# Performance work log

Measured on AMD Instinct MI355X. Metric: run time of the kernel, lower is better.

The kernel has to match this reference:

```python
import jax, jax.numpy as jnp
import numpy as np
from jax import lax

B, C, L = 32, 8, 4096
K, S = 128, 64  # num_shapelets, shapelets_size


def setup_inputs() -> dict:
    key = jax.random.key(0)
    kx, ks = jax.random.split(key)
    x = jax.random.normal(kx, (B, C, L), dtype=jnp.float32)
    shapelets = jax.random.normal(ks, (C, K, S), dtype=jnp.float32)
    return {"x": x, "shapelets": shapelets}


def reference(x, shapelets):
    # x: (B, C, L); shapelets: (C, K, S)
    # Equivalent to: unfold -> cdist(p=2) -> sum over channels -> min over windows.
    # Use the ||a-b||^2 = ||a||^2 + ||b||^2 - 2 a.b expansion so the unfolded
    # (B, C, W, S) tensor is never materialized; cross-terms via grouped conv.
    Bc, Cc, Lc = x.shape
    _, Kc, Sc = shapelets.shape
    dn = ("NCH", "OIH", "NCH")
    # cross[b, c*K+k, w] = sum_s x[b,c,w+s] * shapelets[c,k,s]
    rhs = shapelets.reshape(Cc * Kc, 1, Sc)
    cross = lax.conv_general_dilated(x, rhs, (1,), "VALID",
                                     feature_group_count=Cc,
                                     dimension_numbers=dn)  # (B, C*K, W)
    W = cross.shape[-1]
    cross = cross.reshape(Bc, Cc, Kc, W)
    # sliding window squared norms of x: conv of x^2 with ones kernel per channel
    ones = jnp.ones((Cc, 1, Sc), x.dtype)
    xnorm = lax.conv_general_dilated(x * x, ones, (1,), "VALID",
                                     feature_group_count=Cc,
                                     dimension_numbers=dn)  # (B, C, W)
    snorm = jnp.sum(shapelets * shapelets, axis=-1)  # (C, K)
    d2 = xnorm[:, :, None, :] + snorm[None, :, :, None] - 2.0 * cross  # (B,C,K,W)
    d = jnp.sqrt(jnp.maximum(d2, 1e-12))
    summed = jnp.sum(d, axis=1, keepdims=True)  # (B, 1, K, W)
    return jnp.min(summed, axis=3)  # (B, 1, K)
```

## Files before the change

### kernel.cpp

```cpp
#include <hip/hip_runtime.h>


typedef short short8 __attribute__((ext_vector_type(8)));
typedef float f32x4 __attribute__((ext_vector_type(4)));

constexpr int Bn = 32, Cn = 8, Ln = 4096, Kn = 128, Sn = 64;
constexpr int Wn = Ln - Sn + 1;
constexpr int WT = 128;
constexpr int NWT = (Wn + WT - 1) / WT;
constexpr int BDIM = 256;

typedef const __attribute__((address_space(1))) unsigned int gas_u32;
typedef __attribute__((address_space(3))) unsigned int las_u32;

__device__ __forceinline__ unsigned int f2bf(float f) {
  unsigned int u = __float_as_uint(f);
  u += 0x7FFFu + ((u >> 16) & 1u);
  return u >> 16;
}

__global__ void prep_kernel(const float* __restrict__ sh,
                            unsigned int* __restrict__ out,
                            unsigned short* __restrict__ hbf,
                            float* __restrict__ snorm) {
  int gid = blockIdx.x * blockDim.x + threadIdx.x;
  out[gid] = 0x7F7FFFFFu;
  if (gid < Cn * Kn) {
    const float4* row = (const float4*)(sh + (size_t)gid * Sn);
    char* rowb = (char*)hbf + (size_t)gid * (Sn * 2);
    const unsigned int sw = (gid & 7u) << 4;
    float a = 0.f;
    #pragma unroll
    for (int i = 0; i < 16; ++i) {
      float4 v = row[i];
      a += v.x * v.x + v.y * v.y + v.z * v.z + v.w * v.w;
      unsigned int p0 = f2bf(-2.f * v.x) | (f2bf(-2.f * v.y) << 16);
      unsigned int p1 = f2bf(-2.f * v.z) | (f2bf(-2.f * v.w) << 16);
      *(uint2*)(rowb + ((8u * i) ^ sw)) = make_uint2(p0, p1);
    }
    snorm[gid] = a;
  }
}

__launch_bounds__(BDIM, 2)
__global__ void med_kernel(const float* __restrict__ x,
                           const unsigned short* __restrict__ hbf,
                           const float* __restrict__ snorm,
                           unsigned int* __restrict__ out) {
  constexpr int XRS = 200;
  __shared__ __align__(16) unsigned short Xr[2][8 * XRS];
  __shared__ __align__(16) unsigned short Bs[2][Kn * Sn];
  __shared__ __align__(16) float xnormC[Cn * WT];
  __shared__ __align__(16) float snormC[Cn * Kn];

  const int tid  = threadIdx.x;
  const int b    = blockIdx.y;
  const int w0   = blockIdx.x * WT;
  const int lane = tid & 63;
  const int wv   = tid >> 6;
  const int quad = lane >> 4;
  const int n16  = lane & 15;
  const int wbase = wv * 32;

  const float* xb = x + (size_t)b * Cn * Ln;

  auto stage_b = [&](int bufi, int c) {
    const char* src = (const char*)hbf + (size_t)c * (Kn * Sn * 2);
    char* dst = (char*)&Bs[bufi][0];
    #pragma unroll
    for (int rep = 0; rep < 4; ++rep) {
      int q16 = (tid + rep * BDIM) * 16;
      __builtin_amdgcn_global_load_lds((gas_u32*)(src + q16), (las_u32*)(dst + q16),
                                       16, 0, 0);
    }
  };

  int x_lds[3], x_g[3];
  #pragma unroll
  for (int rep = 0; rep < 3; ++rep) {
    int pid = tid + rep * BDIM;
    int r = pid / 96;
    int p = pid - r * 96;
    x_lds[rep] = r * XRS + 2 * p;
    x_g[rep] = w0 + r + 2 * p;
  }
  float xf[3][2];
  auto load_x = [&](int c) {
    const float* xc = xb + (size_t)c * Ln;
    #pragma unroll
    for (int rep = 0; rep < 3; ++rep) {
      int i0 = x_g[rep];
      xf[rep][0] = (i0 < Ln) ? xc[i0] : 0.f;
      xf[rep][1] = (i0 + 1 < Ln) ? xc[i0 + 1] : 0.f;
    }
  };
  auto write_x = [&](int bufi) {
    #pragma unroll
    for (int rep = 0; rep < 3; ++rep)
      *(unsigned int*)(&Xr[bufi][x_lds[rep]]) =
          f2bf(xf[rep][0]) | (f2bf(xf[rep][1]) << 16);
  };

  ((float4*)snormC)[tid] = ((const float4*)snorm)[tid];

  stage_b(0, 0);
  load_x(0);

  {
    int c  = tid >> 5;
    int m0 = (tid & 31) * 4;
    const float* xc = xb + c * Ln;
    auto xq = [&](int i) -> float {
      float v = (i < Ln) ? xc[i] : 0.f;
      return v * v;
    };
    float s0 = 0.f;
    for (int s = 0; s < Sn; ++s) s0 += xq(w0 + m0 + s);
    float s1 = s0 - xq(w0 + m0 + 0) + xq(w0 + m0 + 64);
    float s2 = s1 - xq(w0 + m0 + 1) + xq(w0 + m0 + 65);
    float s3 = s2 - xq(w0 + m0 + 2) + xq(w0 + m0 + 66);
    xnormC[c * WT + m0 + 0] = s0;
    xnormC[c * WT + m0 + 1] = s1;
    xnormC[c * WT + m0 + 2] = s2;
    xnormC[c * WT + m0 + 3] = s3;
  }
  write_x(0);
  __syncthreads();

  float dist[2][8][4] = {};

  for (int c = 0; c < Cn; ++c) {
    const int buf = c & 1;

    if (c + 1 < Cn) {
      stage_b(buf ^ 1, c + 1);
      load_x(c + 1);
    }

    float4 xn[2];
    #pragma unroll
    for (int mt = 0; mt < 2; ++mt)
      xn[mt] = *(const float4*)(&xnormC[c * WT + wbase + mt * 16 + quad * 4]);

    short8 af[2][2];
    #pragma unroll
    for (int mt = 0; mt < 2; ++mt)
      #pragma unroll
      for (int ks = 0; ks < 2; ++ks) {
        int i = wbase + mt * 16 + n16 + ks * 32 + quad * 8;
        af[mt][ks] = *(const short8*)(&Xr[buf][(i & 7) * XRS + (i >> 3) * 8]);
      }

    const char* bsb = (const char*)&Bs[buf][0];
    #pragma unroll
    for (int pass = 0; pass < 2; ++pass) {
      #pragma unroll
      for (int nt = 0; nt < 4; ++nt) {
        int ksh = pass * 64 + nt * 16 + n16;
        float sn = snormC[c * Kn + ksh];
        int boff = (ksh * 128 + quad * 16) ^ ((ksh & 7) << 4);
        short8 b0 = *(const short8*)(bsb + (boff ^ 0));
        short8 b1 = *(const short8*)(bsb + (boff ^ 64));
        #pragma unroll
        for (int mt = 0; mt < 2; ++mt) {
          f32x4 acc;
          #pragma unroll
          for (int rg = 0; rg < 4; ++rg) acc[rg] = xn[mt][rg] + sn;
          acc = __builtin_amdgcn_mfma_f32_16x16x32_bf16(af[mt][0], b0, acc, 0, 0, 0);
          acc = __builtin_amdgcn_mfma_f32_16x16x32_bf16(af[mt][1], b1, acc, 0, 0, 0);
          #pragma unroll
          for (int rg = 0; rg < 4; ++rg)
            dist[mt][pass * 4 + nt][rg] += __builtin_amdgcn_sqrtf(acc[rg]);
        }
      }
    }

    if (c + 1 < Cn) write_x(buf ^ 1);
    __syncthreads();
  }

  const int wql = w0 + wbase + quad * 4;
  #pragma unroll
  for (int nt2 = 0; nt2 < 8; ++nt2) {
    float v = 3.4e38f;
    #pragma unroll
    for (int mt = 0; mt < 2; ++mt)
      #pragma unroll
      for (int rg = 0; rg < 4; ++rg) {
        int wg = wql + mt * 16 + rg;
        float d = (wg < Wn) ? dist[mt][nt2][rg] : 3.4e38f;
        v = fminf(v, d);
      }
    v = fminf(v, __shfl_xor(v, 16, 64));
    v = fminf(v, __shfl_xor(v, 32, 64));
    if (lane < 16)
      atomicMin(&out[b * Kn + nt2 * 16 + n16], __float_as_uint(v));
  }
}

extern "C" void kernel_launch(void* const* d_in, const int* in_sizes, int n_in,
                              void* d_out, int out_size, void* d_ws, size_t ws_size,
                              hipStream_t stream) {
  const float* x  = (const float*)d_in[0];
  const float* sh = (const float*)d_in[1];
  unsigned int* out = (unsigned int*)d_out;
  unsigned short* hbf = (unsigned short*)d_ws;
  float* snorm = (float*)((char*)d_ws + (size_t)Cn * Kn * Sn * 2);
  hipLaunchKernelGGL(prep_kernel, dim3(16), dim3(256), 0, stream, sh, out, hbf, snorm);
  hipLaunchKernelGGL(med_kernel, dim3(NWT, Bn), dim3(BDIM), 0, stream, x, hbf, snorm, out);
}
```

Baseline: 110.4 us.

## Halve window tile and split shapelet halves across waves for higher occupancy

Shrinks the per-block window tile from 128 to 64. The four waves are now split as 2 window rows × 2 shapelet halves instead of 4 window rows that each cover all 128 shapelets. This halves the per-wave accumulator registers and lets launch bounds request 3 blocks per SIMD, with twice as many blocks in the grid. The trade-off is that every block still stages the full bf16 shapelet matrix per channel, so shapelet LDS and global traffic per output window roughly doubles, and the sliding-norm prologue overhead is amortised over fewer windows.

```diff
diff --git a/kernel.cpp b/kernel.cpp
--- a/kernel.cpp
+++ b/kernel.cpp
@@ -6,9 +6,12 @@
 
 constexpr int Bn = 32, Cn = 8, Ln = 4096, Kn = 128, Sn = 64;
 constexpr int Wn = Ln - Sn + 1;
-constexpr int WT = 128;
+constexpr int WT = 64;
 constexpr int NWT = (Wn + WT - 1) / WT;
 constexpr int BDIM = 256;
+constexpr int XRS = 136;
+constexpr int PPR = 64;
+constexpr int PAIRS = 8 * PPR;
 
 typedef const __attribute__((address_space(1))) unsigned int gas_u32;
 typedef __attribute__((address_space(3))) unsigned int las_u32;
@@ -42,12 +45,11 @@
   }
 }
 
-__launch_bounds__(BDIM, 2)
+__launch_bounds__(BDIM, 3)
 __global__ void med_kernel(const float* __restrict__ x,
                            const unsigned short* __restrict__ hbf,
                            const float* __restrict__ snorm,
                            unsigned int* __restrict__ out) {
-  constexpr int XRS = 200;
   __shared__ __align__(16) unsigned short Xr[2][8 * XRS];
   __shared__ __align__(16) unsigned short Bs[2][Kn * Sn];
   __shared__ __align__(16) float xnormC[Cn * WT];
@@ -60,7 +62,9 @@
   const int wv   = tid >> 6;
   const int quad = lane >> 4;
   const int n16  = lane & 15;
-  const int wbase = wv * 32;
+  const int wrow = wv & 1;
+  const int kh   = wv >> 1;
+  const int wbase = wrow * 32;
 
   const float* xb = x + (size_t)b * Cn * Ln;
 
@@ -75,20 +79,20 @@
     }
   };
 
-  int x_lds[3], x_g[3];
+  int x_lds[2], x_g[2];
   #pragma unroll
-  for (int rep = 0; rep < 3; ++rep) {
+  for (int rep = 0; rep < 2; ++rep) {
     int pid = tid + rep * BDIM;
-    int r = pid / 96;
-    int p = pid - r * 96;
+    int r = pid >> 6;
+    int p = pid & 63;
     x_lds[rep] = r * XRS + 2 * p;
     x_g[rep] = w0 + r + 2 * p;
   }
-  float xf[3][2];
+  float xf[2][2];
   auto load_x = [&](int c) {
     const float* xc = xb + (size_t)c * Ln;
     #pragma unroll
-    for (int rep = 0; rep < 3; ++rep) {
+    for (int rep = 0; rep < 2; ++rep) {
       int i0 = x_g[rep];
       xf[rep][0] = (i0 < Ln) ? xc[i0] : 0.f;
       xf[rep][1] = (i0 + 1 < Ln) ? xc[i0 + 1] : 0.f;
@@ -96,7 +100,7 @@
   };
   auto write_x = [&](int bufi) {
     #pragma unroll
-    for (int rep = 0; rep < 3; ++rep)
+    for (int rep = 0; rep < 2; ++rep)
       *(unsigned int*)(&Xr[bufi][x_lds[rep]]) =
           f2bf(xf[rep][0]) | (f2bf(xf[rep][1]) << 16);
   };
@@ -108,7 +112,7 @@
 
   {
     int c  = tid >> 5;
-    int m0 = (tid & 31) * 4;
+    int m0 = (tid & 31) * 2;
     const float* xc = xb + c * Ln;
     auto xq = [&](int i) -> float {
       float v = (i < Ln) ? xc[i] : 0.f;
@@ -117,17 +121,13 @@
     float s0 = 0.f;
     for (int s = 0; s < Sn; ++s) s0 += xq(w0 + m0 + s);
     float s1 = s0 - xq(w0 + m0 + 0) + xq(w0 + m0 + 64);
-    float s2 = s1 - xq(w0 + m0 + 1) + xq(w0 + m0 + 65);
-    float s3 = s2 - xq(w0 + m0 + 2) + xq(w0 + m0 + 66);
     xnormC[c * WT + m0 + 0] = s0;
     xnormC[c * WT + m0 + 1] = s1;
-    xnormC[c * WT + m0 + 2] = s2;
-    xnormC[c * WT + m0 + 3] = s3;
   }
   write_x(0);
   __syncthreads();
 
-  float dist[2][8][4] = {};
+  float dist[2][4][4] = {};
 
   for (int c = 0; c < Cn; ++c) {
     const int buf = c & 1;
@@ -137,41 +137,32 @@
       load_x(c + 1);
     }
 
-    float4 xn[2];
-    #pragma unroll
-    for (int mt = 0; mt < 2; ++mt)
-      xn[mt] = *(const float4*)(&xnormC[c * WT + wbase + mt * 16 + quad * 4]);
-
-    short8 af[2][2];
-    #pragma unroll
-    for (int mt = 0; mt < 2; ++mt)
-      #pragma unroll
-      for (int ks = 0; ks < 2; ++ks) {
-        int i = wbase + mt * 16 + n16 + ks * 32 + quad * 8;
-        af[mt][ks] = *(const short8*)(&Xr[buf][(i & 7) * XRS + (i >> 3) * 8]);
+    const char* bsb = (const char*)&Bs[buf][0];
+    #pragma unroll
+    for (int mt = 0; mt < 2; ++mt) {
+      float4 xn = *(const float4*)(&xnormC[c * WT + wbase + mt * 16 + quad * 4]);
+      short8 a0, a1;
+      {
+        int i0 = wbase + mt * 16 + n16 + quad * 8;
+        a0 = *(const short8*)(&Xr[buf][(i0 & 7) * XRS + (i0 >> 3) * 8]);
+        int i1 = i0 + 32;
+        a1 = *(const short8*)(&Xr[buf][(i1 & 7) * XRS + (i1 >> 3) * 8]);
       }
-
-    const char* bsb = (const char*)&Bs[buf][0];
-    #pragma unroll
-    for (int pass = 0; pass < 2; ++pass) {
       #pragma unroll
       for (int nt = 0; nt < 4; ++nt) {
-        int ksh = pass * 64 + nt * 16 + n16;
+        int ksh = kh * 64 + nt * 16 + n16;
         float sn = snormC[c * Kn + ksh];
         int boff = (ksh * 128 + quad * 16) ^ ((ksh & 7) << 4);
         short8 b0 = *(const short8*)(bsb + (boff ^ 0));
         short8 b1 = *(const short8*)(bsb + (boff ^ 64));
+        f32x4 acc;
         #pragma unroll
-        for (int mt = 0; mt < 2; ++mt) {
-          f32x4 acc;
-          #pragma unroll
-          for (int rg = 0; rg < 4; ++rg) acc[rg] = xn[mt][rg] + sn;
-          acc = __builtin_amdgcn_mfma_f32_16x16x32_bf16(af[mt][0], b0, acc, 0, 0, 0);
-          acc = __builtin_amdgcn_mfma_f32_16x16x32_bf16(af[mt][1], b1, acc, 0, 0, 0);
-          #pragma unroll
-          for (int rg = 0; rg < 4; ++rg)
-            dist[mt][pass * 4 + nt][rg] += __builtin_amdgcn_sqrtf(acc[rg]);
-        }
+        for (int rg = 0; rg < 4; ++rg) acc[rg] = xn[rg] + sn;
+        acc = __builtin_amdgcn_mfma_f32_16x16x32_bf16(a0, b0, acc, 0, 0, 0);
+        acc = __builtin_amdgcn_mfma_f32_16x16x32_bf16(a1, b1, acc, 0, 0, 0);
+        #pragma unroll
+        for (int rg = 0; rg < 4; ++rg)
+          dist[mt][nt][rg] += __builtin_amdgcn_sqrtf(acc[rg]);
       }
     }
 
@@ -181,20 +172,20 @@
 
   const int wql = w0 + wbase + quad * 4;
   #pragma unroll
-  for (int nt2 = 0; nt2 < 8; ++nt2) {
+  for (int nt = 0; nt < 4; ++nt) {
     float v = 3.4e38f;
     #pragma unroll
     for (int mt = 0; mt < 2; ++mt)
       #pragma unroll
       for (int rg = 0; rg < 4; ++rg) {
         int wg = wql + mt * 16 + rg;
-        float d = (wg < Wn) ? dist[mt][nt2][rg] : 3.4e38f;
+        float d = (wg < Wn) ? dist[mt][nt][rg] : 3.4e38f;
         v = fminf(v, d);
       }
     v = fminf(v, __shfl_xor(v, 16, 64));
     v = fminf(v, __shfl_xor(v, 32, 64));
     if (lane < 16)
-      atomicMin(&out[b * Kn + nt2 * 16 + n16], __float_as_uint(v));
+      atomicMin(&out[b * Kn + kh * 64 + nt * 16 + n16], __float_as_uint(v));
   }
 }
 
```

After: 112.4 us. About the same (+1.8%).
